# Performance work log

Hardware: AMD Instinct MI355X
Metric: run time of the kernel (lower is better)

## Reference

```python
import jax, jax.numpy as jnp
import numpy as np

B, SEQ, PRED, CIN, COUT = 4, 3584, 512, 7, 7
L = SEQ + PRED              # 4096, divisible by 2*BS -> fit_length is a no-op
D, H, DH, FF, EL = 512, 8, 64, 2048, 2
BS, NHASH = 64, 4           # bucket_size, n_hashes
NB = L // BS                # 64 buckets per hash round
SELF_ATTN_VAL = -5e4        # reformer_pytorch TOKEN_SELF_ATTN_VALUE


def layer_norm(x, g, b, eps=1e-5):
    m = jnp.mean(x, -1, keepdims=True)
    v = jnp.mean((x - m) ** 2, -1, keepdims=True)
    return (x - m) * jax.lax.rsqrt(v + eps) * g + b


def lsh_attention(qk, v, rot):
    # qk, v: (bh, L, DH); rot: (DH, NHASH, NB//2)  (shared across batch & heads)
    bh, Lx, dh = qk.shape
    nb = Lx // BS
    # --- hash vectors ---
    rv = jnp.einsum('btf,fhi->bhti', qk, rot)              # (bh, NHASH, L, nb//2)
    rv = jnp.concatenate([rv, -rv], axis=-1)
    buckets = jnp.argmax(rv, axis=-1)                      # (bh, NHASH, L) int
    buckets = buckets + (jnp.arange(NHASH) * nb)[None, :, None]
    buckets = buckets.reshape(bh, NHASH * Lx)
    ticker = jnp.arange(NHASH * Lx)
    bt = Lx * buckets + (ticker % Lx)[None]                # unique keys
    # --- sort by (bucket, position) ---
    sticker = jnp.argsort(bt, axis=-1)                     # (bh, NHASH*L)
    undo = jnp.argsort(sticker, axis=-1)
    st = sticker % Lx
    sqk = jnp.take_along_axis(qk, st[..., None], axis=1)   # (bh, NHASH*L, DH)
    sv = jnp.take_along_axis(v, st[..., None], axis=1)
    ch = NHASH * nb                                        # number of chunks
    bq_t = st.reshape(bh, ch, BS)
    bqk = sqk.reshape(bh, ch, BS, dh)
    bv = sv.reshape(bh, ch, BS, dh)
    bq = bqk
    nrm = jnp.sqrt(jnp.sum(bqk * bqk, -1, keepdims=True))
    bk = bqk / jnp.maximum(nrm, 1e-12)                     # F.normalize
    def look_one_back(t):
        prev = jnp.concatenate([t[:, -1:], t[:, :-1]], axis=1)
        return jnp.concatenate([t, prev], axis=2)
    bk = look_one_back(bk)
    bvv = look_one_back(bv)
    bkv_t = look_one_back(bq_t)
    dots = jnp.einsum('bcie,bcje->bcij', bq, bk) * (dh ** -0.5)  # (bh, ch, BS, 2BS)
    self_mask = bq_t[..., :, None] == bkv_t[..., None, :]
    dots = jnp.where(self_mask, SELF_ATTN_VAL, dots)
    lse = jax.scipy.special.logsumexp(dots, axis=-1, keepdims=True)
    p = jnp.exp(dots - lse)
    bo = jnp.einsum('bcij,bcje->bcie', p, bvv)
    so = bo.reshape(bh, NHASH * Lx, dh)
    slog = lse.reshape(bh, NHASH * Lx)
    o = jnp.take_along_axis(so, undo[..., None], axis=1)
    logits = jnp.take_along_axis(slog, undo, axis=1)
    o = o.reshape(bh, NHASH, Lx, dh)
    logits = logits.reshape(bh, NHASH, Lx, 1)
    probs = jnp.exp(logits - jax.scipy.special.logsumexp(logits, axis=1, keepdims=True))
    return jnp.sum(o * probs, axis=1)                      # (bh, L, DH)


def lsh_self_attention(x, Wqk, Wv, Wo, bo, rot):
    Bs, Lx, _ = x.shape
    qk = (x @ Wqk).reshape(Bs, Lx, H, DH).transpose(0, 2, 1, 3).reshape(Bs * H, Lx, DH)
    v = (x @ Wv).reshape(Bs, Lx, H, DH).transpose(0, 2, 1, 3).reshape(Bs * H, Lx, DH)
    out = lsh_attention(qk, v, rot)
    out = out.reshape(Bs, H, Lx, DH).transpose(0, 2, 1, 3).reshape(Bs, Lx, D)
    return out @ Wo + bo


def _forward(x_enc, x_dec, x_mark_enc, x_mark_dec, conv_w, month_emb, day_emb,
             weekday_emb, hour_emb, minute_emb, W_qk, W_v, W_out, b_out, rotations,
             ln1_g, ln1_b, W_ff1, b_ff1, W_ff2, b_ff2, ln2_g, ln2_b, lnf_g, lnf_b,
             W_proj, b_proj):
    x = jnp.concatenate([x_enc, x_dec[:, -PRED:, :]], axis=1)            # (B, L, CIN)
    xm = jnp.concatenate([x_mark_enc, x_mark_dec[:, -PRED:, :]], axis=1)
    # TokenEmbedding: Conv1d k=3, circular padding, no bias
    xp = jnp.concatenate([x[:, -1:], x, x[:, :1]], axis=1)
    tok = jax.lax.conv_general_dilated(xp, conv_w, (1,), 'VALID',
                                       dimension_numbers=('NWC', 'WIO', 'NWC'))
    # TemporalEmbedding (freq='t': month/day/weekday/hour/minute)
    temp = (month_emb[xm[..., 0]] + day_emb[xm[..., 1]] + weekday_emb[xm[..., 2]]
            + hour_emb[xm[..., 3]] + minute_emb[xm[..., 4]])
    # PositionalEmbedding (sinusoidal)
    pos = jnp.arange(L, dtype=jnp.float32)[:, None]
    div = jnp.exp(jnp.arange(0, D, 2, dtype=jnp.float32) * (-np.log(10000.0) / D))
    pe = jnp.zeros((L, D), jnp.float32).at[:, 0::2].set(jnp.sin(pos * div)).at[:, 1::2].set(jnp.cos(pos * div))
    h = tok + temp + pe[None]
    for l in range(EL):
        a = lsh_self_attention(h, W_qk[l], W_v[l], W_out[l], b_out[l], rotations[l])
        h = layer_norm(h + a, ln1_g[l], ln1_b[l])
        y = jax.nn.gelu(h @ W_ff1[l] + b_ff1[l], approximate=False)
        y = y @ W_ff2[l] + b_ff2[l]
        h = layer_norm(h + y, ln2_g[l], ln2_b[l])
    h = layer_norm(h, lnf_g, lnf_b)
    return h[:, -PRED:] @ W_proj + b_proj                  # (B, PRED, COUT)


def setup_inputs():
    ks = jax.random.split(jax.random.key(0), 20)
    def n(k, shape, fan_in):
        return jax.random.normal(k, shape, jnp.float32) / np.sqrt(fan_in)
    return {
        'x_enc': jax.random.normal(ks[0], (B, SEQ, CIN), jnp.float32),
        'x_dec': jax.random.normal(ks[1], (B, PRED, CIN), jnp.float32),
        'x_mark_enc': jax.random.randint(ks[2], (B, SEQ, 5), 0, 4, jnp.int32),
        'x_mark_dec': jax.random.randint(ks[3], (B, PRED, 5), 0, 4, jnp.int32),
        'conv_w': n(ks[4], (3, CIN, D), 3 * CIN),
        'month_emb': 0.02 * jax.random.normal(ks[5], (13, D), jnp.float32),
        'day_emb': 0.02 * jax.random.normal(ks[6], (32, D), jnp.float32),
        'weekday_emb': 0.02 * jax.random.normal(ks[7], (7, D), jnp.float32),
        'hour_emb': 0.02 * jax.random.normal(ks[8], (24, D), jnp.float32),
        'minute_emb': 0.02 * jax.random.normal(ks[9], (4, D), jnp.float32),
        'W_qk': n(ks[10], (EL, D, D), D),
        'W_v': n(ks[11], (EL, D, D), D),
        'W_out': n(ks[12], (EL, D, D), D),
        'b_out': jnp.zeros((EL, D), jnp.float32),
        'rotations': jax.random.normal(ks[13], (EL, DH, NHASH, NB // 2), jnp.float32),
        'ln1_g': jnp.ones((EL, D), jnp.float32),
        'ln1_b': jnp.zeros((EL, D), jnp.float32),
        'W_ff1': n(ks[14], (EL, D, FF), D),
        'b_ff1': jnp.zeros((EL, FF), jnp.float32),
        'W_ff2': n(ks[15], (EL, FF, D), FF),
        'b_ff2': jnp.zeros((EL, D), jnp.float32),
        'ln2_g': jnp.ones((EL, D), jnp.float32),
        'ln2_b': jnp.zeros((EL, D), jnp.float32),
        'lnf_g': jnp.ones((D,), jnp.float32),
        'lnf_b': jnp.zeros((D,), jnp.float32),
        'W_proj': n(ks[16], (D, COUT), D),
        'b_proj': jnp.zeros((COUT,), jnp.float32),
    }


def reference(x_enc, x_dec, x_mark_enc, x_mark_dec, conv_w, month_emb, day_emb,
              weekday_emb, hour_emb, minute_emb, W_qk, W_v, W_out, b_out, rotations,
              ln1_g, ln1_b, W_ff1, b_ff1, W_ff2, b_ff2, ln2_g, ln2_b, lnf_g, lnf_b,
              W_proj, b_proj):
    return _forward(x_enc, x_dec, x_mark_enc, x_mark_dec, conv_w, month_emb, day_emb,
                    weekday_emb, hour_emb, minute_emb, W_qk, W_v, W_out, b_out, rotations,
                    ln1_g, ln1_b, W_ff1, b_ff1, W_ff2, b_ff2, ln2_g, ln2_b, lnf_g, lnf_b,
                    W_proj, b_proj)
```

## Files before the change

### kernel.cpp

```cpp
#include <hip/hip_runtime.h>
#include <math.h>


typedef __attribute__((ext_vector_type(8))) __bf16 bf16x8;
typedef __attribute__((ext_vector_type(4))) float floatx4;

__device__ __forceinline__ unsigned short f2bf(float f) {
  union { float f; unsigned int u; } x; x.f = f;
  unsigned int r = x.u + 0x7fffu + ((x.u >> 16) & 1u);
  return (unsigned short)(r >> 16);
}
__device__ __forceinline__ float bf2f(unsigned short u) {
  union { unsigned int u; float f; } x; x.u = ((unsigned int)u) << 16;
  return x.f;
}
__device__ __forceinline__ float gelu_f(float x) {
  return 0.5f * x * (1.0f + erff(x * 0.70710678118654752440f));
}

__global__ __launch_bounds__(256) void pe_kernel(float* __restrict__ pe)
{
  int t = blockIdx.x;
#pragma unroll
  for (int rep = 0; rep < 2; ++rep) {
    int d = threadIdx.x + rep * 256;
    float cf = (float)(-9.210340371976184 / 512.0);
    float xf = (float)(d & ~1) * cf;
    float freq = (float)exp((double)xf);
    float angf = (float)t * freq;
    double a = (double)angf;
    pe[t * 512 + d] = (float)((d & 1) ? cos(a) : sin(a));
  }
}

__global__ __launch_bounds__(256) void embed_kernel(
    const float* __restrict__ x_enc, const float* __restrict__ x_dec,
    const int* __restrict__ xm_enc, const int* __restrict__ xm_dec,
    const float* __restrict__ conv_w,
    const float* __restrict__ month, const float* __restrict__ day,
    const float* __restrict__ wday, const float* __restrict__ hour,
    const float* __restrict__ minute, const float* __restrict__ pe,
    float* __restrict__ h)
{
  int idx = blockIdx.x;
  int b = idx >> 12, t = idx & 4095;
  __shared__ float xv[21];
  __shared__ int mi[5];
  int tid = threadIdx.x;
  if (tid < 21) {
    int w = tid / 7, c = tid % 7;
    int s = (t + w + 4095) & 4095;
    xv[tid] = (s < 3584) ? x_enc[(s + b*3584)*7 + c]
                         : x_dec[((s - 3584) + b*512)*7 + c];
  }
  if (tid >= 32 && tid < 37) {
    int j = tid - 32;
    mi[j] = (t < 3584) ? xm_enc[(b*3584 + t)*5 + j]
                       : xm_dec[(b*512 + (t - 3584))*5 + j];
  }
  __syncthreads();
  int m0 = mi[0], m1 = mi[1], m2 = mi[2], m3 = mi[3], m4 = mi[4];
#pragma unroll
  for (int rep = 0; rep < 2; ++rep) {
    int d = tid + rep*256;
    float tok = 0.f;
#pragma unroll
    for (int wc = 0; wc < 21; ++wc) tok += xv[wc] * conv_w[wc*512 + d];
    float temp = month[m0*512+d] + day[m1*512+d] + wday[m2*512+d]
               + hour[m3*512+d] + minute[m4*512+d];
    h[(size_t)idx*512 + d] = tok + temp + pe[t*512 + d];
  }
}

template<int ACT>
__global__ __launch_bounds__(256) void gemm_kernel(
    const float* __restrict__ A, const float* __restrict__ W,
    const float* __restrict__ bias, float* __restrict__ C,
    int M, int N, int K)
{
  __shared__ float As[8][132];
  __shared__ float Bs[8][132];
  int tid = threadIdx.x;
  int bm = blockIdx.x, bn = blockIdx.y;
  int tr = tid >> 4, tc = tid & 15;
  double acc[8][8];
  float tt[8][8];
#pragma unroll
  for (int i=0;i<8;++i)
#pragma unroll
    for (int j=0;j<8;++j) { acc[i][j]=0.0; tt[i][j]=0.f; }

  int am  = tid >> 1;
  int at  = (tid & 1) * 4;
  int bkr = tid >> 5;
  int bn4 = (tid & 31) * 4;
  const float* Aptr = A + (size_t)(bm*128 + am)*K + at;
  const float* Bptr = W + (size_t)bkr*N + bn*128 + bn4;

  int phase = 0;
  for (int k0 = 0; k0 < K; k0 += 8) {
    float4 a4 = *(const float4*)(Aptr + k0);
    float4 b4 = *(const float4*)(Bptr + (size_t)k0*N);
    __syncthreads();
    As[at+0][am] = a4.x; As[at+1][am] = a4.y;
    As[at+2][am] = a4.z; As[at+3][am] = a4.w;
    *(float4*)&Bs[bkr][bn4] = b4;
    __syncthreads();
#pragma unroll
    for (int k=0;k<8;++k) {
      float4 a0 = *(const float4*)&As[k][tr*8];
      float4 a1 = *(const float4*)&As[k][tr*8+4];
      float4 b0 = *(const float4*)&Bs[k][tc*8];
      float4 b1 = *(const float4*)&Bs[k][tc*8+4];
      float av[8] = {a0.x,a0.y,a0.z,a0.w,a1.x,a1.y,a1.z,a1.w};
      float bv[8] = {b0.x,b0.y,b0.z,b0.w,b1.x,b1.y,b1.z,b1.w};
#pragma unroll
      for (int i=0;i<8;++i)
#pragma unroll
        for (int j=0;j<8;++j) tt[i][j] += av[i]*bv[j];
    }
    phase ^= 1;
    if (!phase) {
#pragma unroll
      for (int i=0;i<8;++i)
#pragma unroll
        for (int j=0;j<8;++j) { acc[i][j] += (double)tt[i][j]; tt[i][j]=0.f; }
    }
  }
  int row0 = bm*128 + tr*8;
  int col0 = bn*128 + tc*8;
  float bvb[8];
#pragma unroll
  for (int j=0;j<8;++j) bvb[j] = bias ? bias[col0+j] : 0.f;
#pragma unroll
  for (int i=0;i<8;++i) {
    float o[8];
#pragma unroll
    for (int j=0;j<8;++j) {
      float vv = (float)acc[i][j] + bvb[j];
      if (ACT==1) vv = gelu_f(vv);
      o[j] = vv;
    }
    float4* dst = (float4*)(C + (size_t)(row0+i)*N + col0);
    dst[0] = make_float4(o[0],o[1],o[2],o[3]);
    dst[1] = make_float4(o[4],o[5],o[6],o[7]);
  }
}

template<int SPLIT>
__global__ __launch_bounds__(256) void wsplit_kernel(
    const float* __restrict__ W, unsigned short* __restrict__ Wt, int K, int N)
{
  __shared__ float tile[32][33];
  int k0 = blockIdx.x*32, n0 = blockIdx.y*32;
  int tid = threadIdx.x;
  int kk = tid >> 3, nn4 = (tid & 7)*4;
  float4 w4 = *(const float4*)(W + (size_t)(k0+kk)*N + n0 + nn4);
  tile[kk][nn4+0]=w4.x; tile[kk][nn4+1]=w4.y;
  tile[kk][nn4+2]=w4.z; tile[kk][nn4+3]=w4.w;
  __syncthreads();
  int n = tid >> 3, k4 = (tid & 7)*4;
  unsigned short o[3][4];
#pragma unroll
  for (int j=0;j<4;++j) {
    float v = tile[k4+j][n];
    unsigned short h0 = f2bf(v);
    float r = v - bf2f(h0);
    unsigned short h1 = f2bf(r);
    o[0][j] = h0; o[1][j] = h1;
    if (SPLIT==3) { float r2 = r - bf2f(h1); o[2][j] = f2bf(r2); }
  }
#pragma unroll
  for (int p=0;p<SPLIT;++p) {
    ushort4* d = (ushort4*)(Wt + (size_t)p*N*K + (size_t)(n0+n)*K + k0 + k4);
    *d = make_ushort4(o[p][0], o[p][1], o[p][2], o[p][3]);
  }
}

template<int SPLIT, int ACT>
__global__ __launch_bounds__(256) void gemm_mfma(
    const float* __restrict__ A, const unsigned short* __restrict__ Wt,
    const float* __restrict__ bias, float* __restrict__ C,
    int M, int N, int K)
{
  constexpr int LDK = 40;
  __shared__ __align__(16) unsigned short sA[SPLIT*128*LDK];
  __shared__ __align__(16) unsigned short sB[SPLIT*128*LDK];
  int tid = threadIdx.x;
  int bm = blockIdx.x, bn = blockIdx.y;
  int lane = tid & 63, wave = tid >> 6;
  int wm = wave & 1, wn = wave >> 1;
  int fr = lane & 15, fk = (lane >> 4) * 8;

  floatx4 acc[4][4];
#pragma unroll
  for (int i=0;i<4;++i)
#pragma unroll
    for (int j=0;j<4;++j) acc[i][j] = (floatx4){0.f,0.f,0.f,0.f};

  int row = tid >> 1, kseg = (tid & 1) * 16;
  const float* aSrc = A + (size_t)(bm*128 + row)*K + kseg;
  const unsigned short* bSrc = Wt + (size_t)(bn*128 + row)*K + kseg;

  for (int k0 = 0; k0 < K; k0 += 32) {
    float4 av4[4];
#pragma unroll
    for (int q=0;q<4;++q) av4[q] = *(const float4*)(aSrc + k0 + q*4);
    uint4 bv[SPLIT][2];
#pragma unroll
    for (int p=0;p<SPLIT;++p) {
      const unsigned short* bp = bSrc + (size_t)p*N*K + k0;
      bv[p][0] = *(const uint4*)(bp);
      bv[p][1] = *(const uint4*)(bp + 8);
    }
    __syncthreads();
    unsigned short us[3][16];
    const float* ff = (const float*)av4;
#pragma unroll
    for (int i=0;i<16;++i) {
      float v = ff[i];
      unsigned short h0 = f2bf(v);
      float r = v - bf2f(h0);
      unsigned short h1 = f2bf(r);
      us[0][i] = h0; us[1][i] = h1;
      if (SPLIT==3) { float r2 = r - bf2f(h1); us[2][i] = f2bf(r2); }
    }
#pragma unroll
    for (int p=0;p<SPLIT;++p) {
      uint4* d = (uint4*)&sA[p*128*LDK + row*LDK + kseg];
      d[0] = *(const uint4*)&us[p][0];
      d[1] = *(const uint4*)&us[p][8];
    }
#pragma unroll
    for (int p=0;p<SPLIT;++p) {
      uint4* d = (uint4*)&sB[p*128*LDK + row*LDK + kseg];
      d[0] = bv[p][0];
      d[1] = bv[p][1];
    }
    __syncthreads();

    bf16x8 aF[4][SPLIT];
#pragma unroll
    for (int mt=0;mt<4;++mt)
#pragma unroll
      for (int p=0;p<SPLIT;++p)
        aF[mt][p] = *(const bf16x8*)&sA[p*128*LDK + (wm*64 + mt*16 + fr)*LDK + fk];
#pragma unroll
    for (int nt=0;nt<4;++nt) {
      bf16x8 bF[SPLIT];
#pragma unroll
      for (int p=0;p<SPLIT;++p)
        bF[p] = *(const bf16x8*)&sB[p*128*LDK + (wn*64 + nt*16 + fr)*LDK + fk];
#pragma unroll
      for (int mt=0;mt<4;++mt) {
        floatx4 c = acc[mt][nt];
        if (SPLIT==3) {
          c = __builtin_amdgcn_mfma_f32_16x16x32_bf16(aF[mt][2], bF[0], c, 0,0,0);
          c = __builtin_amdgcn_mfma_f32_16x16x32_bf16(aF[mt][1], bF[1], c, 0,0,0);
          c = __builtin_amdgcn_mfma_f32_16x16x32_bf16(aF[mt][0], bF[2], c, 0,0,0);
        }
        c = __builtin_amdgcn_mfma_f32_16x16x32_bf16(aF[mt][1], bF[0], c, 0,0,0);
        c = __builtin_amdgcn_mfma_f32_16x16x32_bf16(aF[mt][0], bF[1], c, 0,0,0);
        c = __builtin_amdgcn_mfma_f32_16x16x32_bf16(aF[mt][0], bF[0], c, 0,0,0);
        acc[mt][nt] = c;
      }
    }
  }
#pragma unroll
  for (int nt=0;nt<4;++nt) {
    int gc = bn*128 + wn*64 + nt*16 + fr;
    float bb = bias ? bias[gc] : 0.f;
#pragma unroll
    for (int mt=0;mt<4;++mt) {
      int gr0 = bm*128 + wm*64 + mt*16 + (lane>>4)*4;
#pragma unroll
      for (int r=0;r<4;++r) {
        float vv = acc[mt][nt][r] + bb;
        if (ACT==1) vv = gelu_f(vv);
        C[(size_t)(gr0 + r)*N + gc] = vv;
      }
    }
  }
}

__global__ __launch_bounds__(256) void hash_kernel(
    const float* __restrict__ qk, const float* __restrict__ rot,
    unsigned char* __restrict__ buckets)
{
  __shared__ float q[2][64];
  __shared__ double rv[2][128];
  int half = threadIdx.x >> 7;
  int lt = threadIdx.x & 127;
  int g = blockIdx.x*2 + half;
  int bh = g >> 12, t = g & 4095;
  int b = bh >> 3, hd = bh & 7;
  if (lt < 64)
    q[half][lt] = qk[((size_t)(b*4096 + t))*512 + hd*64 + lt];
  __syncthreads();
  double acc = 0.0;
#pragma unroll 8
  for (int f=0; f<64; ++f) acc += (double)q[half][f] * (double)rot[f*128 + lt];
  rv[half][lt] = acc;
  __syncthreads();
  if (lt < 4) {
    const double* r = &rv[half][lt*32];
    double best = r[0]; int bi = 0;
#pragma unroll
    for (int j=1; j<64; ++j) {
      double v = (j < 32) ? r[j] : -r[j-32];
      if (v > best) { best = v; bi = j; }
    }
    buckets[((size_t)(bh*4 + lt))*4096 + t] = (unsigned char)bi;
  }
}

__global__ __launch_bounds__(64) void sort_kernel(
    const unsigned char* __restrict__ buckets, int* __restrict__ st)
{
  __shared__ unsigned char sb[4096];
  __shared__ int cnts[64];
  int tid = threadIdx.x;
  const unsigned int* src4 = (const unsigned int*)(buckets + (size_t)blockIdx.x*4096);
  unsigned int* sb4 = (unsigned int*)sb;
  for (int i=tid; i<1024; i+=64) sb4[i] = src4[i];
  __syncthreads();
  unsigned int me = (unsigned int)tid;
  int cnt = 0;
  for (int t4=0; t4<1024; ++t4) {
    unsigned int w = sb4[t4];
    cnt += ((w & 255u) == me) + (((w>>8)&255u) == me)
         + (((w>>16)&255u) == me) + ((w>>24) == me);
  }
  cnts[tid] = cnt;
  __syncthreads();
  int base = 0;
  for (int j=0;j<tid;++j) base += cnts[j];
  int* dst = st + (size_t)blockIdx.x*4096;
  for (int t4=0; t4<1024; ++t4) {
    unsigned int w = sb4[t4];
#pragma unroll
    for (int q=0;q<4;++q)
      if (((w >> (8*q)) & 255u) == me) dst[base++] = t4*4 + q;
  }
}

__global__ __launch_bounds__(256) void attn_kernel(
    const float* __restrict__ qk, const float* __restrict__ v,
    const int* __restrict__ st, float* __restrict__ osc,
    float* __restrict__ logits)
{
  __shared__ float sMem[8704];
  __shared__ float sPT[128][68];
  __shared__ int sPos[128];
  __shared__ float sInv[128];
  int tid = threadIdx.x;
  int bh = blockIdx.x >> 8;
  int c  = blockIdx.x & 255;
  int b = bh >> 3, hd = bh & 7;
  int r = c >> 6;
  if (tid < 128) {
    int cprev = (c + 255) & 255;
    int slot = (tid < 64) ? (c*64 + tid) : (cprev*64 + tid - 64);
    sPos[tid] = st[bh*16384 + slot];
  }
  __syncthreads();
  {
    int j = tid >> 1;
    int f0 = (tid & 1) * 32;
    const float* row = qk + ((size_t)(b*4096 + sPos[j]))*512 + hd*64 + f0;
#pragma unroll
    for (int qq=0; qq<8; ++qq) {
      float4 x = *(const float4*)(row + qq*4);
      int f = f0 + qq*4;
      sMem[(f+0)*132 + j] = x.x;
      sMem[(f+1)*132 + j] = x.y;
      sMem[(f+2)*132 + j] = x.z;
      sMem[(f+3)*132 + j] = x.w;
    }
  }
  __syncthreads();
  if (tid < 128) {
    float s = 0.f;
    for (int f=0; f<64; ++f) { float x = sMem[f*132 + tid]; s += x*x; }
    sInv[tid] = 1.0f / fmaxf(sqrtf(s), 1e-12f);
  }
  __syncthreads();
  int tr = tid >> 4, tcj = tid & 15;
  int i0 = tr*4, j0 = tcj*8;
  float acc[4][8];
#pragma unroll
  for (int i=0;i<4;++i)
#pragma unroll
    for (int j=0;j<8;++j) acc[i][j]=0.f;
  for (int f=0; f<64; ++f) {
    const float* base = &sMem[f*132];
    float4 a  = *(const float4*)(base + i0);
    float4 b0 = *(const float4*)(base + j0);
    float4 b1 = *(const float4*)(base + j0 + 4);
    float av[4] = {a.x,a.y,a.z,a.w};
    float bw[8] = {b0.x,b0.y,b0.z,b0.w,b1.x,b1.y,b1.z,b1.w};
#pragma unroll
    for (int i=0;i<4;++i)
#pragma unroll
      for (int j=0;j<8;++j) acc[i][j] += av[i]*bw[j];
  }
  float inv_j[8]; int pos_j[8];
#pragma unroll
  for (int j=0;j<8;++j) { inv_j[j] = sInv[j0+j]; pos_j[j] = sPos[j0+j]; }
#pragma unroll
  for (int ii=0; ii<4; ++ii) {
    int i = i0 + ii;
    int ipos = sPos[i];
    float dv[8]; float mx = -1e30f;
#pragma unroll
    for (int jj=0;jj<8;++jj) {
      float d = acc[ii][jj] * inv_j[jj] * 0.125f;
      if (pos_j[jj] == ipos) d = -5.0e4f;
      dv[jj] = d; mx = fmaxf(mx, d);
    }
    mx = fmaxf(mx, __shfl_xor(mx, 1, 64));
    mx = fmaxf(mx, __shfl_xor(mx, 2, 64));
    mx = fmaxf(mx, __shfl_xor(mx, 4, 64));
    mx = fmaxf(mx, __shfl_xor(mx, 8, 64));
    float sum = 0.f;
#pragma unroll
    for (int jj=0;jj<8;++jj) sum += expf(dv[jj]-mx);
    sum += __shfl_xor(sum, 1, 64);
    sum += __shfl_xor(sum, 2, 64);
    sum += __shfl_xor(sum, 4, 64);
    sum += __shfl_xor(sum, 8, 64);
    float lse = mx + logf(sum);
    if (tcj == 0)
      logits[((size_t)(bh*4 + r))*4096 + ipos] = lse;
#pragma unroll
    for (int jj=0;jj<8;++jj)
      sPT[j0+jj][i] = expf(dv[jj]-lse);
  }
  __syncthreads();
  {
    int j = tid >> 1;
    int f0 = (tid & 1) * 32;
    const float* row = v + ((size_t)(b*4096 + sPos[j]))*512 + hd*64 + f0;
#pragma unroll
    for (int qq=0; qq<8; ++qq) {
      float4 x = *(const float4*)(row + qq*4);
      *(float4*)&sMem[j*68 + f0 + qq*4] = x;
    }
  }
  __syncthreads();
  int d0 = (tid & 15) * 4;
  float oo[4][4];
#pragma unroll
  for (int i=0;i<4;++i)
#pragma unroll
    for (int j=0;j<4;++j) oo[i][j]=0.f;
  for (int j = 0; j < 128; ++j) {
    float4 pw = *(const float4*)&sPT[j][i0];
    float4 vv = *(const float4*)&sMem[j*68 + d0];
    float pr[4] = {pw.x, pw.y, pw.z, pw.w};
#pragma unroll
    for (int ii=0; ii<4; ++ii) {
      oo[ii][0] += pr[ii]*vv.x;
      oo[ii][1] += pr[ii]*vv.y;
      oo[ii][2] += pr[ii]*vv.z;
      oo[ii][3] += pr[ii]*vv.w;
    }
  }
#pragma unroll
  for (int ii=0; ii<4; ++ii) {
    int pos = sPos[i0+ii];
    float4* dst = (float4*)(osc + (((size_t)(bh*4+r))*4096 + pos)*64 + d0);
    *dst = make_float4(oo[ii][0],oo[ii][1],oo[ii][2],oo[ii][3]);
  }
}

__global__ __launch_bounds__(256) void combine_kernel(
    const float* __restrict__ osc, const float* __restrict__ logits,
    float* __restrict__ merged)
{
  int idx = blockIdx.x;
  int b = idx >> 12, t = idx & 4095;
  int tid = threadIdx.x;
  __shared__ float w[8][4];
  if (tid < 8) {
    size_t lbase = ((size_t)(b*8 + tid)) * 4 * 4096 + t;
    float l0 = logits[lbase], l1 = logits[lbase + 4096],
          l2 = logits[lbase + 8192], l3 = logits[lbase + 12288];
    float m = fmaxf(fmaxf(l0,l1), fmaxf(l2,l3));
    float e0 = expf(l0-m), e1 = expf(l1-m), e2 = expf(l2-m), e3 = expf(l3-m);
    float inv = 1.0f/(e0+e1+e2+e3);
    w[tid][0]=e0*inv; w[tid][1]=e1*inv; w[tid][2]=e2*inv; w[tid][3]=e3*inv;
  }
  __syncthreads();
#pragma unroll
  for (int rep=0; rep<2; ++rep) {
    int d = tid + rep*256;
    int hd = d >> 6, dh = d & 63;
    size_t obase = (((size_t)(b*8 + hd)) * 4 * 4096 + t) * 64 + dh;
    float o = w[hd][0]*osc[obase]
            + w[hd][1]*osc[obase + 262144]
            + w[hd][2]*osc[obase + 524288]
            + w[hd][3]*osc[obase + 786432];
    merged[(size_t)idx*512 + d] = o;
  }
}

__global__ __launch_bounds__(256) void ln_residual_kernel(
    float* __restrict__ h, const float* __restrict__ a,
    const float* __restrict__ g, const float* __restrict__ bb)
{
  int row = blockIdx.x;
  int tid = threadIdx.x;
  size_t base = (size_t)row * 512;
  float x0 = h[base + tid]       + a[base + tid];
  float x1 = h[base + tid + 256] + a[base + tid + 256];
  float s  = x0 + x1;
  float sq = x0*x0 + x1*x1;
#pragma unroll
  for (int off = 32; off > 0; off >>= 1) {
    s  += __shfl_down(s, off, 64);
    sq += __shfl_down(sq, off, 64);
  }
  __shared__ float rs[4], rq[4], sm[2];
  int wv = tid >> 6;
  if ((tid & 63) == 0) { rs[wv] = s; rq[wv] = sq; }
  __syncthreads();
  if (tid == 0) {
    float S = rs[0]+rs[1]+rs[2]+rs[3];
    float Q = rq[0]+rq[1]+rq[2]+rq[3];
    float m = S * (1.0f/512.0f);
    float var = Q * (1.0f/512.0f) - m*m;
    sm[0] = m; sm[1] = rsqrtf(var + 1e-5f);
  }
  __syncthreads();
  float m = sm[0], rstd = sm[1];
  h[base + tid]       = (x0 - m) * rstd * g[tid]       + bb[tid];
  h[base + tid + 256] = (x1 - m) * rstd * g[tid + 256] + bb[tid + 256];
}

__global__ __launch_bounds__(256) void final_kernel(
    const float* __restrict__ h, const float* __restrict__ g, const float* __restrict__ bb,
    const float* __restrict__ Wp, const float* __restrict__ bp, float* __restrict__ out)
{
  int idx = blockIdx.x;
  int b = idx >> 9, tp = idx & 511;
  size_t base = ((size_t)(b*4096 + 3584 + tp)) * 512;
  int tid = threadIdx.x;
  float x0 = h[base + tid], x1 = h[base + tid + 256];
  float s = x0 + x1, sq = x0*x0 + x1*x1;
#pragma unroll
  for (int off = 32; off > 0; off >>= 1) {
    s  += __shfl_down(s, off, 64);
    sq += __shfl_down(sq, off, 64);
  }
  __shared__ float rs[4], rq[4], sm[2];
  int wv = tid >> 6;
  if ((tid & 63) == 0) { rs[wv] = s; rq[wv] = sq; }
  __syncthreads();
  if (tid == 0) {
    float S = rs[0]+rs[1]+rs[2]+rs[3];
    float Q = rq[0]+rq[1]+rq[2]+rq[3];
    float m = S*(1.f/512.f);
    float var = Q*(1.f/512.f) - m*m;
    sm[0]=m; sm[1]=rsqrtf(var+1e-5f);
  }
  __syncthreads();
  __shared__ float xn[512];
  float m = sm[0], rstd = sm[1];
  xn[tid]     = (x0-m)*rstd*g[tid]     + bb[tid];
  xn[tid+256] = (x1-m)*rstd*g[tid+256] + bb[tid+256];
  __syncthreads();
  if (tid < 224) {
    int col = tid >> 5, lane = tid & 31;
    float p = 0.f;
    for (int f = lane; f < 512; f += 32) p += xn[f]*Wp[f*7 + col];
#pragma unroll
    for (int off=16; off>0; off>>=1) p += __shfl_down(p, off, 32);
    if (lane == 0) out[(size_t)idx*7 + col] = p + bp[col];
  }
}

extern "C" void kernel_launch(void* const* d_in, const int* in_sizes, int n_in,
                              void* d_out, int out_size, void* d_ws, size_t ws_size,
                              hipStream_t stream)
{
  (void)in_sizes; (void)n_in; (void)out_size; (void)ws_size;
  const float* x_enc  = (const float*)d_in[0];
  const float* x_dec  = (const float*)d_in[1];
  const int*   xm_enc = (const int*)d_in[2];
  const int*   xm_dec = (const int*)d_in[3];
  const float* conv_w = (const float*)d_in[4];
  const float* month  = (const float*)d_in[5];
  const float* day    = (const float*)d_in[6];
  const float* wday   = (const float*)d_in[7];
  const float* hourE  = (const float*)d_in[8];
  const float* minE   = (const float*)d_in[9];
  const float* W_qk   = (const float*)d_in[10];
  const float* W_v    = (const float*)d_in[11];
  const float* W_out  = (const float*)d_in[12];
  const float* b_out  = (const float*)d_in[13];
  const float* rots   = (const float*)d_in[14];
  const float* ln1_g  = (const float*)d_in[15];
  const float* ln1_b  = (const float*)d_in[16];
  const float* W_ff1  = (const float*)d_in[17];
  const float* b_ff1  = (const float*)d_in[18];
  const float* W_ff2  = (const float*)d_in[19];
  const float* b_ff2  = (const float*)d_in[20];
  const float* ln2_g  = (const float*)d_in[21];
  const float* ln2_b  = (const float*)d_in[22];
  const float* lnf_g  = (const float*)d_in[23];
  const float* lnf_b  = (const float*)d_in[24];
  const float* W_proj = (const float*)d_in[25];
  const float* b_proj = (const float*)d_in[26];

  float* h    = (float*)d_ws;
  float* bufA = h    + 8388608ull;
  float* bufB = bufA + 8388608ull;
  float* osc  = bufB + 8388608ull;
  float* lg   = osc  + 33554432ull;
  int*   stp  = (int*)(lg + 524288ull);
  unsigned char* bkt = (unsigned char*)(stp + 524288ull);
  float* pe   = osc;
  unsigned short* WtA = (unsigned short*)osc;
  unsigned short* WtB = (unsigned short*)bufB;

  pe_kernel<<<4096, 256, 0, stream>>>(pe);
  embed_kernel<<<16384, 256, 0, stream>>>(x_enc, x_dec, xm_enc, xm_dec, conv_w,
                                          month, day, wday, hourE, minE, pe, h);
  for (int l = 0; l < 2; ++l) {
    const float* Wqk = W_qk + (size_t)l*262144;
    const float* Wv  = W_v  + (size_t)l*262144;
    const float* Wo  = W_out+ (size_t)l*262144;
    const float* Wf1 = W_ff1 + (size_t)l*1048576;
    const float* Wf2 = W_ff2 + (size_t)l*1048576;
    const float* rot = rots + (size_t)l*8192;

    gemm_kernel<0><<<dim3(128,4), 256, 0, stream>>>(h, Wqk, nullptr, bufA, 16384, 512, 512);
    if (l == 0) {
      wsplit_kernel<3><<<dim3(16,16), 256, 0, stream>>>(Wv, WtA, 512, 512);
      gemm_mfma<3,0><<<dim3(128,4), 256, 0, stream>>>(h, WtA, nullptr, bufB, 16384, 512, 512);
    } else {
      wsplit_kernel<2><<<dim3(16,16), 256, 0, stream>>>(Wv, WtA, 512, 512);
      gemm_mfma<2,0><<<dim3(128,4), 256, 0, stream>>>(h, WtA, nullptr, bufB, 16384, 512, 512);
    }
    hash_kernel<<<65536, 256, 0, stream>>>(bufA, rot, bkt);
    sort_kernel<<<128, 64, 0, stream>>>(bkt, stp);
    attn_kernel<<<8192, 256, 0, stream>>>(bufA, bufB, stp, osc, lg);
    combine_kernel<<<16384, 256, 0, stream>>>(osc, lg, bufA);
    if (l == 0) {
      wsplit_kernel<3><<<dim3(16,16), 256, 0, stream>>>(Wo, WtA, 512, 512);
      gemm_mfma<3,0><<<dim3(128,4), 256, 0, stream>>>(bufA, WtA, b_out + l*512, bufB, 16384, 512, 512);
    } else {
      wsplit_kernel<2><<<dim3(16,16), 256, 0, stream>>>(Wo, WtA, 512, 512);
      gemm_mfma<2,0><<<dim3(128,4), 256, 0, stream>>>(bufA, WtA, b_out + l*512, bufB, 16384, 512, 512);
    }
    ln_residual_kernel<<<16384, 256, 0, stream>>>(h, bufB, ln1_g + l*512, ln1_b + l*512);
    if (l == 0) {
      wsplit_kernel<3><<<dim3(16,64), 256, 0, stream>>>(Wf1, WtB, 512, 2048);
      gemm_mfma<3,1><<<dim3(128,16), 256, 0, stream>>>(h, WtB, b_ff1 + l*2048, osc, 16384, 2048, 512);
      wsplit_kernel<3><<<dim3(64,16), 256, 0, stream>>>(Wf2, WtB, 2048, 512);
      gemm_mfma<3,0><<<dim3(128,4), 256, 0, stream>>>(osc, WtB, b_ff2 + l*512, bufA, 16384, 512, 2048);
    } else {
      wsplit_kernel<2><<<dim3(16,64), 256, 0, stream>>>(Wf1, WtB, 512, 2048);
      gemm_mfma<2,1><<<dim3(128,16), 256, 0, stream>>>(h, WtB, b_ff1 + l*2048, osc, 16384, 2048, 512);
      wsplit_kernel<2><<<dim3(64,16), 256, 0, stream>>>(Wf2, WtB, 2048, 512);
      gemm_mfma<2,0><<<dim3(128,4), 256, 0, stream>>>(osc, WtB, b_ff2 + l*512, bufA, 16384, 512, 2048);
    }
    ln_residual_kernel<<<16384, 256, 0, stream>>>(h, bufA, ln2_g + l*512, ln2_b + l*512);
  }
  final_kernel<<<2048, 256, 0, stream>>>(h, lnf_g, lnf_b, W_proj, b_proj, (float*)d_out);
}
```

Before: 3.574 ms.

## Prefetch next GEMM tile into registers, interleave split LDS layout, stage epilogue stores

The global loads for the next K tile are issued right after the LDS barrier, so they overlap with the MFMA work on the current tile. The split bf16 planes are now interleaved per row in a single shared buffer, and occupancy is hinted with launch_bounds(256,3). The epilogue writes results through shared memory in two halves so each row can be stored with coalesced float4 writes instead of scattered scalar stores. The cost is more live registers for the prefetched data and extra barriers in the epilogue.

```diff
diff --git a/kernel.cpp b/kernel.cpp
--- a/kernel.cpp
+++ b/kernel.cpp
@@ -178,14 +178,17 @@
 }
 
 template<int SPLIT, int ACT>
-__global__ __launch_bounds__(256) void gemm_mfma(
+__global__ __launch_bounds__(256, 3) void gemm_mfma(
     const float* __restrict__ A, const unsigned short* __restrict__ Wt,
     const float* __restrict__ bias, float* __restrict__ C,
     int M, int N, int K)
 {
-  constexpr int LDK = 40;
-  __shared__ __align__(16) unsigned short sA[SPLIT*128*LDK];
-  __shared__ __align__(16) unsigned short sB[SPLIT*128*LDK];
+  constexpr int RS = SPLIT*32 + 8;
+  __shared__ __align__(16) unsigned short smem[2*128*RS];
+  unsigned short* sA = smem;
+  unsigned short* sB = smem + 128*RS;
+  float* sE = (float*)smem;
+
   int tid = threadIdx.x;
   int bm = blockIdx.x, bn = blockIdx.y;
   int lane = tid & 63, wave = tid >> 6;
@@ -202,55 +205,64 @@
   const float* aSrc = A + (size_t)(bm*128 + row)*K + kseg;
   const unsigned short* bSrc = Wt + (size_t)(bn*128 + row)*K + kseg;
 
+  float4 av4[4];
+  uint4 bv[SPLIT][2];
+#pragma unroll
+  for (int q=0;q<4;++q) av4[q] = *(const float4*)(aSrc + q*4);
+#pragma unroll
+  for (int p=0;p<SPLIT;++p) {
+    const unsigned short* bp = bSrc + (size_t)p*N*K;
+    bv[p][0] = *(const uint4*)(bp);
+    bv[p][1] = *(const uint4*)(bp + 8);
+  }
+
   for (int k0 = 0; k0 < K; k0 += 32) {
-    float4 av4[4];
-#pragma unroll
-    for (int q=0;q<4;++q) av4[q] = *(const float4*)(aSrc + k0 + q*4);
-    uint4 bv[SPLIT][2];
-#pragma unroll
-    for (int p=0;p<SPLIT;++p) {
-      const unsigned short* bp = bSrc + (size_t)p*N*K + k0;
-      bv[p][0] = *(const uint4*)(bp);
-      bv[p][1] = *(const uint4*)(bp + 8);
-    }
     __syncthreads();
-    unsigned short us[3][16];
+    unsigned short us[SPLIT][16];
     const float* ff = (const float*)av4;
 #pragma unroll
     for (int i=0;i<16;++i) {
       float v = ff[i];
       unsigned short h0 = f2bf(v);
       float r = v - bf2f(h0);
+      us[0][i] = h0;
       unsigned short h1 = f2bf(r);
-      us[0][i] = h0; us[1][i] = h1;
+      us[1][i] = h1;
       if (SPLIT==3) { float r2 = r - bf2f(h1); us[2][i] = f2bf(r2); }
     }
 #pragma unroll
     for (int p=0;p<SPLIT;++p) {
-      uint4* d = (uint4*)&sA[p*128*LDK + row*LDK + kseg];
+      uint4* d = (uint4*)&sA[row*RS + p*32 + kseg];
       d[0] = *(const uint4*)&us[p][0];
       d[1] = *(const uint4*)&us[p][8];
-    }
-#pragma unroll
-    for (int p=0;p<SPLIT;++p) {
-      uint4* d = (uint4*)&sB[p*128*LDK + row*LDK + kseg];
-      d[0] = bv[p][0];
-      d[1] = bv[p][1];
+      uint4* db = (uint4*)&sB[row*RS + p*32 + kseg];
+      db[0] = bv[p][0];
+      db[1] = bv[p][1];
     }
     __syncthreads();
+    if (k0 + 32 < K) {
+#pragma unroll
+      for (int q=0;q<4;++q) av4[q] = *(const float4*)(aSrc + k0 + 32 + q*4);
+#pragma unroll
+      for (int p=0;p<SPLIT;++p) {
+        const unsigned short* bp = bSrc + (size_t)p*N*K + k0 + 32;
+        bv[p][0] = *(const uint4*)(bp);
+        bv[p][1] = *(const uint4*)(bp + 8);
+      }
+    }
 
     bf16x8 aF[4][SPLIT];
 #pragma unroll
     for (int mt=0;mt<4;++mt)
 #pragma unroll
       for (int p=0;p<SPLIT;++p)
-        aF[mt][p] = *(const bf16x8*)&sA[p*128*LDK + (wm*64 + mt*16 + fr)*LDK + fk];
+        aF[mt][p] = *(const bf16x8*)&sA[(wm*64 + mt*16 + fr)*RS + p*32 + fk];
 #pragma unroll
     for (int nt=0;nt<4;++nt) {
       bf16x8 bF[SPLIT];
 #pragma unroll
       for (int p=0;p<SPLIT;++p)
-        bF[p] = *(const bf16x8*)&sB[p*128*LDK + (wn*64 + nt*16 + fr)*LDK + fk];
+        bF[p] = *(const bf16x8*)&sB[(wn*64 + nt*16 + fr)*RS + p*32 + fk];
 #pragma unroll
       for (int mt=0;mt<4;++mt) {
         floatx4 c = acc[mt][nt];
@@ -266,20 +278,36 @@
       }
     }
   }
-#pragma unroll
-  for (int nt=0;nt<4;++nt) {
-    int gc = bn*128 + wn*64 + nt*16 + fr;
-    float bb = bias ? bias[gc] : 0.f;
-#pragma unroll
-    for (int mt=0;mt<4;++mt) {
-      int gr0 = bm*128 + wm*64 + mt*16 + (lane>>4)*4;
-#pragma unroll
-      for (int r=0;r<4;++r) {
-        float vv = acc[mt][nt][r] + bb;
-        if (ACT==1) vv = gelu_f(vv);
-        C[(size_t)(gr0 + r)*N + gc] = vv;
+
+  __syncthreads();
+#pragma unroll
+  for (int half = 0; half < 2; ++half) {
+    if (wm == half) {
+#pragma unroll
+      for (int nt=0;nt<4;++nt) {
+        int cl = wn*64 + nt*16 + fr;
+        float bb = bias ? bias[bn*128 + cl] : 0.f;
+#pragma unroll
+        for (int mt=0;mt<4;++mt) {
+          int r0 = mt*16 + (lane>>4)*4;
+#pragma unroll
+          for (int j=0;j<4;++j) {
+            float vv = acc[mt][nt][j] + bb;
+            if (ACT==1) vv = gelu_f(vv);
+            sE[(r0+j)*132 + cl] = vv;
+          }
+        }
       }
     }
+    __syncthreads();
+#pragma unroll
+    for (int it=0; it<8; ++it) {
+      int idx = it*256 + tid;
+      int rr = idx >> 5, c4 = (idx & 31) * 4;
+      float4 vv = *(const float4*)&sE[rr*132 + c4];
+      *(float4*)(C + (size_t)(bm*128 + half*64 + rr)*N + bn*128 + c4) = vv;
+    }
+    __syncthreads();
   }
 }
 
```

New measurement: 3.565 ms. About the same (-0.2%).
